# Kernel optimization log

Measured on AMD Instinct MI355X. Metric: run time of the kernel, lower is better.

The kernel has to match this reference:

```python
import jax, jax.numpy as jnp
import numpy as np

TAU = 32.0
ALPHA = 0.9
B, C, F = 4096, 512, 128  # batch, n_classes, n_bits


def setup_inputs() -> dict:
    key = jax.random.key(0)
    k1, k2, k3, k4 = jax.random.split(key, 4)
    X = jax.random.normal(k1, (B, F), dtype=jnp.float32)
    T = jax.random.randint(k2, (B, C), 0, 2).astype(jnp.int32)  # 0/1 multi-label
    # kaiming_normal_(mode='fan_out') on a [C, F] tensor -> std = sqrt(2 / C)
    std = np.sqrt(2.0 / C).astype(np.float32)
    means = jax.random.normal(k3, (C, F), dtype=jnp.float32) * std
    log_vars = jax.random.normal(k4, (C, F), dtype=jnp.float32) * std
    return {"X": X, "T": T, "means": means, "log_vars": log_vars}


def _l2_normalize(x, eps=1e-12):
    # matches torch F.normalize(p=2): x / max(||x||, eps)
    n = jnp.sqrt(jnp.sum(x * x, axis=-1, keepdims=True))
    return x / jnp.maximum(n, eps)


def _mahalanobis(Xn, mu, log_vars):
    # M[i,j] = sum_f (x_if - mu_jf)^2 / exp(lv_jf)
    # expanded into three GEMM-like terms -> never materializes [N,C,F]
    inv = jnp.exp(-log_vars)                         # [C, F]
    t1 = (Xn * Xn) @ inv.T                           # [N, C]
    t2 = Xn @ (mu * inv).T                           # [N, C]
    t3 = jnp.sum(mu * mu * inv, axis=-1)             # [C]
    return t1 - 2.0 * t2 + t3[None, :]


def reference(X, T, means, log_vars):
    lv = jnp.clip(log_vars, 0.0, 6.0)                # relu6
    Xn = _l2_normalize(X)
    mu = _l2_normalize(means)
    D = _mahalanobis(Xn, mu, lv)                     # [N, C]

    P_all = jax.nn.softmax(-TAU * D, axis=1)         # [N, C]
    Tf = T.astype(X.dtype)
    P_sum = jnp.sum(P_all * Tf, axis=1)              # [N]
    nz = P_sum != 0
    safe = jnp.where(nz, P_sum, 1.0)
    loss = -jnp.sum(jnp.where(nz, jnp.log(safe), 0.0)) / jnp.maximum(
        jnp.sum(nz).astype(X.dtype), 1.0)

    # classes present in the batch (concrete mask -> static column selection)
    cw = np.asarray(jnp.sum(T, axis=0) != 0)
    Dc = D[:, cw]                                    # [N, Ccw]
    Tc = Tf[:, cw]
    S = Tc + jnp.exp(-ALPHA * Dc) * (1.0 - Tc)
    return (loss, S)
```

## Files before the change

kernel.cpp:

```cpp
#include <hip/hip_runtime.h>
#include <hip/hip_bf16.h>
#include <math.h>

#define NB 4096
#define NC 512
#define NF 128
#define NK 256
#define TAUc 32.0f
#define ALPHAc 0.9f

typedef __attribute__((ext_vector_type(8))) short bf16x8;
typedef __attribute__((ext_vector_type(4))) float f32x4;
typedef __attribute__((address_space(1))) const unsigned int gu32;
typedef __attribute__((address_space(3))) unsigned int lu32;

__device__ inline void splitbf(float x, short& hi, short& lo) {
  unsigned u = __float_as_uint(x);
  hi = (short)(u >> 16);
  float l = x - __uint_as_float(u & 0xFFFF0000u);
  lo = (short)(__float_as_uint(l) >> 16);
}

__global__ __launch_bounds__(128) void k_prepB(const float* __restrict__ means,
                                               const float* __restrict__ logv,
                                               ushort* __restrict__ Bh,
                                               ushort* __restrict__ Bl,
                                               float* __restrict__ t3) {
  __shared__ float p2[2];
  __shared__ float q2[2];
  int c = blockIdx.x, f = threadIdx.x;
  float mu = means[(size_t)c * NF + f];
  float lv = fminf(fmaxf(logv[(size_t)c * NF + f], 0.f), 6.f);
  float iv = __expf(-lv);
  float s = mu * mu;
  #pragma unroll
  for (int o = 1; o < 64; o <<= 1) s += __shfl_xor(s, o, 64);
  if ((f & 63) == 0) p2[f >> 6] = s;
  __syncthreads();
  float mun = mu / fmaxf(sqrtf(p2[0] + p2[1]), 1e-12f);

  int ct = c >> 4, lr = c & 15;
  auto swadr = [&](int k) {
    return (size_t)(ct * 8 + (k >> 5)) * 512 + ((k >> 3) & 3) * 128 + lr * 8 + (k & 7);
  };
  short h, l;
  splitbf(iv, h, l);
  size_t a1 = swadr(f);
  Bh[a1] = (ushort)h; Bl[a1] = (ushort)l;
  splitbf(-2.f * mun * iv, h, l);
  size_t a2 = swadr(f + NF);
  Bh[a2] = (ushort)h; Bl[a2] = (ushort)l;

  float t = mun * mun * iv;
  #pragma unroll
  for (int o = 1; o < 64; o <<= 1) t += __shfl_xor(t, o, 64);
  if ((f & 63) == 0) q2[f >> 6] = t;
  __syncthreads();
  if (f == 0) t3[c] = q2[0] + q2[1];
}

__global__ __launch_bounds__(512) void k_zero(int* __restrict__ colnz) {
  colnz[threadIdx.x] = 0;
}

__global__ __launch_bounds__(256) void k_mask(const int* __restrict__ T,
                                              int* __restrict__ colnz) {
  int r0 = blockIdx.x * 16;
  int a0 = 0, a1 = 0;
  for (int r = 0; r < 16; ++r) {
    const int* row = T + (size_t)(r0 + r) * NC;
    a0 |= row[threadIdx.x];
    a1 |= row[threadIdx.x + 256];
  }
  if (a0) atomicOr(colnz + threadIdx.x, 1);
  if (a1) atomicOr(colnz + threadIdx.x + 256, 1);
}

__global__ __launch_bounds__(512) void k_scan(const int* __restrict__ colnz,
                                              int* __restrict__ pos) {
  __shared__ int s[NC];
  int t = threadIdx.x;
  int f = colnz[t] ? 1 : 0;
  s[t] = f;
  __syncthreads();
  for (int o = 1; o < NC; o <<= 1) {
    int add = (t >= o) ? s[t - o] : 0;
    __syncthreads();
    s[t] += add;
    __syncthreads();
  }
  pos[t] = s[t] - f;
}

__global__ __launch_bounds__(512) void k_fused(const float* __restrict__ X,
                                               const int* __restrict__ T,
                                               const ushort* __restrict__ Bh,
                                               const ushort* __restrict__ Bl,
                                               const float* __restrict__ t3,
                                               const int* __restrict__ colnz,
                                               const int* __restrict__ pos,
                                               float* __restrict__ Sout,
                                               float* __restrict__ blklog,
                                               int* __restrict__ blkcnt,
                                               int Csel, int ident) {
  __shared__ __align__(16) unsigned char smraw[131072];
  __shared__ float sl16[16];
  __shared__ int sc16[16];
  int tid = threadIdx.x;
  int lane = tid & 63, w = tid >> 6;
  int lr = lane & 15, kq = lane >> 4;
  int r0 = blockIdx.x * 16;

  auto stage = [&](int p) {
    int par = p & 1;
    #pragma unroll
    for (int t = 0; t < 4; ++t) {
      size_t goff = (((size_t)(w * 4 + t) * 8 + p) * 64 + lane) * 8;
      unsigned ldso = (unsigned)(w * 16384 + par * 8192 + t * 2048);
      __builtin_amdgcn_global_load_lds((gu32*)(Bh + goff), (lu32*)(smraw + ldso), 16, 0, 0);
      __builtin_amdgcn_global_load_lds((gu32*)(Bl + goff), (lu32*)(smraw + ldso + 1024), 16, 0, 0);
    }
  };
  stage(0);

  float xv[4][8];
  float rsum = 0.f;
  const float* xrow = X + (size_t)(r0 + lr) * NF + 8 * kq;
  #pragma unroll
  for (int c = 0; c < 4; ++c) {
    float4 u0 = *(const float4*)(xrow + 32 * c);
    float4 u1 = *(const float4*)(xrow + 32 * c + 4);
    xv[c][0] = u0.x; xv[c][1] = u0.y; xv[c][2] = u0.z; xv[c][3] = u0.w;
    xv[c][4] = u1.x; xv[c][5] = u1.y; xv[c][6] = u1.z; xv[c][7] = u1.w;
    #pragma unroll
    for (int j = 0; j < 8; ++j) rsum = fmaf(xv[c][j], xv[c][j], rsum);
  }
  rsum += __shfl_xor(rsum, 16, 64);
  rsum += __shfl_xor(rsum, 32, 64);
  float rn = 1.0f / fmaxf(sqrtf(rsum), 1e-12f);

  bf16x8 Afh[8], Afl[8];
  #pragma unroll
  for (int c = 0; c < 4; ++c) {
    #pragma unroll
    for (int j = 0; j < 8; ++j) {
      float xn = xv[c][j] * rn;
      short h, l;
      splitbf(xn * xn, h, l);
      Afh[c][j] = h; Afl[c][j] = l;
      splitbf(xn, h, l);
      Afh[c + 4][j] = h; Afl[c + 4][j] = l;
    }
  }

  int tf0[8], tf1[8];
  {
    const int* Trow0 = T + (size_t)(r0 + 2 * w) * NC;
    const int* Trow1 = T + (size_t)(r0 + 2 * w + 1) * NC;
    #pragma unroll
    for (int j = 0; j < 8; ++j) {
      tf0[j] = Trow0[lane + 64 * j];
      tf1[j] = Trow1[lane + 64 * j];
    }
  }

  const bf16x8* wstage = (const bf16x8*)(smraw + w * 16384);
  f32x4 acc[4] = {};
  #pragma unroll
  for (int k8 = 0; k8 < 8; ++k8) {
    if (k8 < 7) {
      stage(k8 + 1);
      asm volatile("s_waitcnt vmcnt(8)" ::: "memory");
    } else {
      asm volatile("s_waitcnt vmcnt(0)" ::: "memory");
    }
    int par = k8 & 1;
    #pragma unroll
    for (int t = 0; t < 4; ++t) {
      bf16x8 bh = wstage[(par * 8 + t * 2) * 64 + lane];
      bf16x8 bl = wstage[(par * 8 + t * 2 + 1) * 64 + lane];
      acc[t] = __builtin_amdgcn_mfma_f32_16x16x32_bf16(Afh[k8], bh, acc[t], 0, 0, 0);
      acc[t] = __builtin_amdgcn_mfma_f32_16x16x32_bf16(Afl[k8], bh, acc[t], 0, 0, 0);
      acc[t] = __builtin_amdgcn_mfma_f32_16x16x32_bf16(Afh[k8], bl, acc[t], 0, 0, 0);
    }
  }
  __syncthreads();

  float (*Dls)[514] = (float (*)[514])smraw;
  int n0 = w * 64;
  #pragma unroll
  for (int t = 0; t < 4; ++t) {
    int c = n0 + 16 * t + lr;
    float tt = t3[c];
    #pragma unroll
    for (int i = 0; i < 4; ++i) Dls[4 * kq + i][c] = acc[t][i] + tt;
  }
  __syncthreads();

  #pragma unroll
  for (int rr = 0; rr < 2; ++rr) {
    int r = 2 * w + rr;
    const int* tf = rr ? tf1 : tf0;
    float d[8];
    #pragma unroll
    for (int j = 0; j < 8; ++j) d[j] = Dls[r][lane + 64 * j];
    float dmin = d[0];
    #pragma unroll
    for (int j = 1; j < 8; ++j) dmin = fminf(dmin, d[j]);
    #pragma unroll
    for (int o = 1; o < 64; o <<= 1) dmin = fminf(dmin, __shfl_xor(dmin, o, 64));
    float Z = 0.f, Ps = 0.f;
    #pragma unroll
    for (int j = 0; j < 8; ++j) {
      float p = __expf(TAUc * (dmin - d[j]));
      Z += p;
      if (tf[j]) Ps += p;
    }
    #pragma unroll
    for (int o = 1; o < 64; o <<= 1) { Z += __shfl_xor(Z, o, 64); Ps += __shfl_xor(Ps, o, 64); }
    float* srow = Sout + (size_t)(r0 + r) * Csel;
    if (ident) {
      #pragma unroll
      for (int j = 0; j < 8; ++j)
        srow[lane + 64 * j] = tf[j] ? 1.0f : __expf(-ALPHAc * d[j]);
    } else {
      #pragma unroll
      for (int j = 0; j < 8; ++j) {
        int c = lane + 64 * j;
        if (colnz[c]) srow[pos[c]] = tf[j] ? 1.0f : __expf(-ALPHAc * d[j]);
      }
    }
    if (lane == 0) {
      float Psum = Ps / Z;
      sl16[r] = (Psum > 0.f) ? logf(Psum) : 0.f;
      sc16[r] = (Psum > 0.f) ? 1 : 0;
    }
  }
  __syncthreads();
  if (tid == 0) {
    float s = 0.f; int c = 0;
    #pragma unroll
    for (int r = 0; r < 16; ++r) { s += sl16[r]; c += sc16[r]; }
    blklog[blockIdx.x] = s;
    blkcnt[blockIdx.x] = c;
  }
}

__global__ __launch_bounds__(256) void k_fin(const float* __restrict__ blklog,
                                             const int* __restrict__ blkcnt,
                                             float* __restrict__ out) {
  __shared__ float sl[256];
  __shared__ int sc[256];
  int t = threadIdx.x;
  sl[t] = blklog[t];
  sc[t] = blkcnt[t];
  __syncthreads();
  for (int o = 128; o > 0; o >>= 1) {
    if (t < o) { sl[t] += sl[t + o]; sc[t] += sc[t + o]; }
    __syncthreads();
  }
  if (t == 0) out[0] = -sl[0] / fmaxf((float)sc[0], 1.0f);
}

extern "C" void kernel_launch(void* const* d_in, const int* in_sizes, int n_in,
                              void* d_out, int out_size, void* d_ws, size_t ws_size,
                              hipStream_t stream) {
  const float* X     = (const float*)d_in[0];
  const int*   T     = (const int*)d_in[1];
  const float* means = (const float*)d_in[2];
  const float* logv  = (const float*)d_in[3];
  float* out = (float*)d_out;
  char* ws = (char*)d_ws;

  ushort* Bh      = (ushort*)(ws);
  ushort* Bl      = (ushort*)(ws + 262144);
  float*  t3      = (float*) (ws + 524288);
  float*  blklog  = (float*) (ws + 526336);
  int*    blkcnt  = (int*)   (ws + 527360);
  int*    colnz   = (int*)   (ws + 528384);
  int*    pos     = (int*)   (ws + 530432);

  int Csel = (out_size - 1) / NB;
  int ident = (Csel == NC);

  k_prepB<<<NC, NF, 0, stream>>>(means, logv, Bh, Bl, t3);
  if (!ident) {
    k_zero<<<1, NC, 0, stream>>>(colnz);
    k_mask<<<NB / 16, 256, 0, stream>>>(T, colnz);
    k_scan<<<1, NC, 0, stream>>>(colnz, pos);
  }
  k_fused<<<NB / 16, 512, 0, stream>>>(X, T, Bh, Bl, t3, colnz, pos,
                                       out + 1, blklog, blkcnt, Csel, ident);
  k_fin<<<1, 256, 0, stream>>>(blklog, blkcnt, out);
}
```

Baseline: 23.75 us.

## Merge prep, main and final reduction into one cooperative kernel with grid syncs

Folds the B-matrix preparation and the final loss reduction into the main fused kernel and launches it cooperatively, with grid-wide syncs between the phases. This removes two extra kernel launches and the gaps between them. In exchange it adds two grid barriers, and it requires all 256 blocks of 512 threads with 128KB of LDS each to be co-resident, one per CU.

```diff
diff --git a/kernel.cpp b/kernel.cpp
--- a/kernel.cpp
+++ b/kernel.cpp
@@ -1,6 +1,9 @@
 #include <hip/hip_runtime.h>
+#include <hip/hip_cooperative_groups.h>
 #include <hip/hip_bf16.h>
 #include <math.h>
+
+namespace cg = cooperative_groups;
 
 #define NB 4096
 #define NC 512
@@ -19,44 +22,6 @@
   hi = (short)(u >> 16);
   float l = x - __uint_as_float(u & 0xFFFF0000u);
   lo = (short)(__float_as_uint(l) >> 16);
-}
-
-__global__ __launch_bounds__(128) void k_prepB(const float* __restrict__ means,
-                                               const float* __restrict__ logv,
-                                               ushort* __restrict__ Bh,
-                                               ushort* __restrict__ Bl,
-                                               float* __restrict__ t3) {
-  __shared__ float p2[2];
-  __shared__ float q2[2];
-  int c = blockIdx.x, f = threadIdx.x;
-  float mu = means[(size_t)c * NF + f];
-  float lv = fminf(fmaxf(logv[(size_t)c * NF + f], 0.f), 6.f);
-  float iv = __expf(-lv);
-  float s = mu * mu;
-  #pragma unroll
-  for (int o = 1; o < 64; o <<= 1) s += __shfl_xor(s, o, 64);
-  if ((f & 63) == 0) p2[f >> 6] = s;
-  __syncthreads();
-  float mun = mu / fmaxf(sqrtf(p2[0] + p2[1]), 1e-12f);
-
-  int ct = c >> 4, lr = c & 15;
-  auto swadr = [&](int k) {
-    return (size_t)(ct * 8 + (k >> 5)) * 512 + ((k >> 3) & 3) * 128 + lr * 8 + (k & 7);
-  };
-  short h, l;
-  splitbf(iv, h, l);
-  size_t a1 = swadr(f);
-  Bh[a1] = (ushort)h; Bl[a1] = (ushort)l;
-  splitbf(-2.f * mun * iv, h, l);
-  size_t a2 = swadr(f + NF);
-  Bh[a2] = (ushort)h; Bl[a2] = (ushort)l;
-
-  float t = mun * mun * iv;
-  #pragma unroll
-  for (int o = 1; o < 64; o <<= 1) t += __shfl_xor(t, o, 64);
-  if ((f & 63) == 0) q2[f >> 6] = t;
-  __syncthreads();
-  if (f == 0) t3[c] = q2[0] + q2[1];
 }
 
 __global__ __launch_bounds__(512) void k_zero(int* __restrict__ colnz) {
@@ -92,23 +57,69 @@
   pos[t] = s[t] - f;
 }
 
-__global__ __launch_bounds__(512) void k_fused(const float* __restrict__ X,
-                                               const int* __restrict__ T,
-                                               const ushort* __restrict__ Bh,
-                                               const ushort* __restrict__ Bl,
-                                               const float* __restrict__ t3,
-                                               const int* __restrict__ colnz,
-                                               const int* __restrict__ pos,
-                                               float* __restrict__ Sout,
-                                               float* __restrict__ blklog,
-                                               int* __restrict__ blkcnt,
-                                               int Csel, int ident) {
+__global__ __launch_bounds__(512) void k_mono(const float* __restrict__ X,
+                                              const int* __restrict__ T,
+                                              const float* __restrict__ means,
+                                              const float* __restrict__ logv,
+                                              ushort* __restrict__ Bh,
+                                              ushort* __restrict__ Bl,
+                                              float* __restrict__ t3,
+                                              const int* __restrict__ colnz,
+                                              const int* __restrict__ pos,
+                                              float* __restrict__ out,
+                                              float* __restrict__ blklog,
+                                              int* __restrict__ blkcnt,
+                                              int Csel, int ident) {
   __shared__ __align__(16) unsigned char smraw[131072];
   __shared__ float sl16[16];
   __shared__ int sc16[16];
+  __shared__ float ph1[8];
   int tid = threadIdx.x;
   int lane = tid & 63, w = tid >> 6;
   int lr = lane & 15, kq = lane >> 4;
+
+  {
+    float mu = 0.f, iv = 0.f;
+    int c = blockIdx.x * 2 + (tid >> 7);
+    int f = tid & 127;
+    if (tid < 256) {
+      mu = means[(size_t)c * NF + f];
+      float lv = fminf(fmaxf(logv[(size_t)c * NF + f], 0.f), 6.f);
+      iv = __expf(-lv);
+      float s = mu * mu;
+      #pragma unroll
+      for (int o = 1; o < 64; o <<= 1) s += __shfl_xor(s, o, 64);
+      if (lane == 0) ph1[w] = s;
+    }
+    __syncthreads();
+    if (tid < 256) {
+      int half = tid >> 7;
+      float tot = ph1[half * 2] + ph1[half * 2 + 1];
+      float mun = mu / fmaxf(sqrtf(tot), 1e-12f);
+      int ct = c >> 4, clr = c & 15;
+      auto swadr = [&](int k) {
+        return (size_t)(ct * 8 + (k >> 5)) * 512 + ((k >> 3) & 3) * 128 + clr * 8 + (k & 7);
+      };
+      short h, l;
+      splitbf(iv, h, l);
+      size_t a1 = swadr(f);
+      Bh[a1] = (ushort)h; Bl[a1] = (ushort)l;
+      splitbf(-2.f * mun * iv, h, l);
+      size_t a2 = swadr(f + NF);
+      Bh[a2] = (ushort)h; Bl[a2] = (ushort)l;
+      float t = mun * mun * iv;
+      #pragma unroll
+      for (int o = 1; o < 64; o <<= 1) t += __shfl_xor(t, o, 64);
+      if (lane == 0) ph1[4 + w] = t;
+    }
+    __syncthreads();
+    if (tid < 256 && (tid & 127) == 0) {
+      int half = tid >> 7;
+      t3[blockIdx.x * 2 + half] = ph1[4 + half * 2] + ph1[4 + half * 2 + 1];
+    }
+  }
+  cg::this_grid().sync();
+
   int r0 = blockIdx.x * 16;
 
   auto stage = [&](int p) {
@@ -218,7 +229,7 @@
     }
     #pragma unroll
     for (int o = 1; o < 64; o <<= 1) { Z += __shfl_xor(Z, o, 64); Ps += __shfl_xor(Ps, o, 64); }
-    float* srow = Sout + (size_t)(r0 + r) * Csel;
+    float* srow = out + 1 + (size_t)(r0 + r) * Csel;
     if (ident) {
       #pragma unroll
       for (int j = 0; j < 8; ++j)
@@ -243,23 +254,21 @@
     for (int r = 0; r < 16; ++r) { s += sl16[r]; c += sc16[r]; }
     blklog[blockIdx.x] = s;
     blkcnt[blockIdx.x] = c;
-  }
-}
-
-__global__ __launch_bounds__(256) void k_fin(const float* __restrict__ blklog,
-                                             const int* __restrict__ blkcnt,
-                                             float* __restrict__ out) {
-  __shared__ float sl[256];
-  __shared__ int sc[256];
-  int t = threadIdx.x;
-  sl[t] = blklog[t];
-  sc[t] = blkcnt[t];
-  __syncthreads();
-  for (int o = 128; o > 0; o >>= 1) {
-    if (t < o) { sl[t] += sl[t + o]; sc[t] += sc[t + o]; }
-    __syncthreads();
-  }
-  if (t == 0) out[0] = -sl[0] / fmaxf((float)sc[0], 1.0f);
+    __threadfence();
+  }
+  cg::this_grid().sync();
+
+  if (blockIdx.x == 0) {
+    float* rf = (float*)smraw;
+    int*   ri = (int*)(smraw + 2048);
+    if (tid < 256) { rf[tid] = blklog[tid]; ri[tid] = blkcnt[tid]; }
+    __syncthreads();
+    for (int o = 128; o > 0; o >>= 1) {
+      if (tid < o) { rf[tid] += rf[tid + o]; ri[tid] += ri[tid + o]; }
+      __syncthreads();
+    }
+    if (tid == 0) out[0] = -rf[0] / fmaxf((float)ri[0], 1.0f);
+  }
 }
 
 extern "C" void kernel_launch(void* const* d_in, const int* in_sizes, int n_in,
@@ -283,13 +292,17 @@
   int Csel = (out_size - 1) / NB;
   int ident = (Csel == NC);
 
-  k_prepB<<<NC, NF, 0, stream>>>(means, logv, Bh, Bl, t3);
   if (!ident) {
     k_zero<<<1, NC, 0, stream>>>(colnz);
     k_mask<<<NB / 16, 256, 0, stream>>>(T, colnz);
     k_scan<<<1, NC, 0, stream>>>(colnz, pos);
   }
-  k_fused<<<NB / 16, 512, 0, stream>>>(X, T, Bh, Bl, t3, colnz, pos,
-                                       out + 1, blklog, blkcnt, Csel, ident);
-  k_fin<<<1, 256, 0, stream>>>(blklog, blkcnt, out);
-}
+
+  void* args[] = { (void*)&X, (void*)&T, (void*)&means, (void*)&logv,
+                   (void*)&Bh, (void*)&Bl, (void*)&t3,
+                   (void*)&colnz, (void*)&pos,
+                   (void*)&out, (void*)&blklog, (void*)&blkcnt,
+                   (void*)&Csel, (void*)&ident };
+  hipLaunchCooperativeKernel((const void*)k_mono, dim3(NB / 16), dim3(512),
+                             args, 0, stream);
+}
```

Measured after the change: 78.81 us. 3.32x slower.
